# Performance work log

Measured on AMD Instinct MI355X. Metric: run time of the kernel, lower is better.

The kernel has to match this reference:

```python
import jax, jax.numpy as jnp
import numpy as np

N, C, H, W = 4, 15, 320, 320
FEATS_OUT, KSIZE, PAD, CONV_PAD, K_RBF = 32, 11, 11, 5, 31
VMAX = 1.0


def _fft2c(x):
    # fastMRI-style centered orthonormal 2D FFT on complex array [..., H, W]
    x = jnp.fft.ifftshift(x, axes=(-2, -1))
    x = jnp.fft.fft2(x, axes=(-2, -1), norm='ortho')
    return jnp.fft.fftshift(x, axes=(-2, -1))


def _ifft2c(x):
    x = jnp.fft.ifftshift(x, axes=(-2, -1))
    x = jnp.fft.ifft2(x, axes=(-2, -1), norm='ortho')
    return jnp.fft.fftshift(x, axes=(-2, -1))


def _to_c(x):
    return jax.lax.complex(x[..., 0], x[..., 1])


def _to_r(z):
    return jnp.stack([jnp.real(z), jnp.imag(z)], axis=-1)


def setup_inputs() -> dict:
    key = jax.random.key(0)
    ks = jax.random.split(key, 8)
    u_t = jax.random.normal(ks[0], (N, H, W, 2), dtype=jnp.float32)
    f = jax.random.normal(ks[1], (N, C, H, W, 2), dtype=jnp.float32)
    coil_sens = jax.random.normal(ks[2], (N, C, H, W, 2), dtype=jnp.float32)
    sampling_mask = (jax.random.uniform(ks[3], (N, H, W)) < 0.35).astype(jnp.float32)
    conv_kernel = jax.random.normal(ks[4], (FEATS_OUT, 1, KSIZE, KSIZE, 2), dtype=jnp.float32)
    conv_kernel = conv_kernel / np.sqrt(KSIZE * KSIZE * 2 * 1)
    conv_kernel = conv_kernel - jnp.mean(conv_kernel, axis=(1, 2, 3, 4), keepdims=True)
    x0 = jnp.linspace(-VMAX, VMAX, K_RBF, dtype=jnp.float32)
    w = jnp.broadcast_to((0.04 * x0).reshape(1, 1, 1, 1, K_RBF), (1, FEATS_OUT, 1, 1, K_RBF)).astype(jnp.float32)
    mu = x0
    sigma = jnp.array([2.0 * VMAX / (K_RBF - 1)], dtype=jnp.float32)
    lamb = jnp.array([1.0], dtype=jnp.float32)
    return {'u_t': u_t, 'f': f, 'coil_sens': coil_sens, 'sampling_mask': sampling_mask,
            'conv_kernel': conv_kernel, 'w': w, 'mu': mu, 'sigma': sigma, 'lamb': lamb}


def reference(u_t, f, coil_sens, sampling_mask, conv_kernel, w, mu, sigma, lamb):
    dn = ('NCHW', 'OIHW', 'NCHW')
    feats_out = conv_kernel.shape[0]
    k = conv_kernel.shape[2]

    # --- regularizer: reflect-pad, complex conv pair, RBF activation, transposed conv pair ---
    pad_cfg = ((0, 0), (0, 0), (PAD, PAD), (PAD, PAD))
    ur = jnp.pad(u_t[:, None, :, :, 0], pad_cfg, mode='reflect')  # [N,1,Hp,Wp]
    ui = jnp.pad(u_t[:, None, :, :, 1], pad_cfg, mode='reflect')

    def conv(x, Wk):
        return jax.lax.conv_general_dilated(x, Wk, (1, 1), [(CONV_PAD, CONV_PAD)] * 2,
                                            dimension_numbers=dn)

    u_k = conv(ur, conv_kernel[..., 0]) + conv(ui, conv_kernel[..., 1])  # [N,Co,Hp,Wp]

    # RBF activation: sum_i w_i * exp(-(x - mu_i)^2 / (2 sigma^2)), scanned over centers
    wk = jnp.transpose(w[0, :, 0, 0, :])  # [K, Co]
    inv2s2 = 1.0 / (2.0 * sigma[0] ** 2)

    def body(acc, wm):
        wi, mi = wm
        acc = acc + wi[None, :, None, None] * jnp.exp(-jnp.square(u_k - mi) * inv2s2)
        return acc, None

    f_u_k, _ = jax.lax.scan(body, jnp.zeros_like(u_k), (wk, mu))

    # conv_transpose2d(padding=CONV_PAD) == conv with flipped kernel, swapped channels, padding k-1-CONV_PAD
    tpad = k - 1 - CONV_PAD

    def convT(x, Wk):
        Wt = jnp.transpose(Wk[:, :, ::-1, ::-1], (1, 0, 2, 3))  # [I,O,k,k] -> OIHW w/ O=1
        return jax.lax.conv_general_dilated(x, Wt, (1, 1), [(tpad, tpad)] * 2,
                                            dimension_numbers=dn)

    Ru_r = convT(f_u_k, conv_kernel[..., 0])[:, 0]  # [N,Hp,Wp]
    Ru_i = convT(f_u_k, conv_kernel[..., 1])[:, 0]
    Ru = jnp.stack([Ru_r, Ru_i], axis=-1)[:, PAD:-PAD, PAD:-PAD, :] / feats_out  # [N,H,W,2]

    # --- data consistency: A^T (A u - f) (cartesian, os=False) ---
    u_c = _to_c(u_t)              # [N,H,W]
    c_c = _to_c(coil_sens)        # [N,C,H,W]
    f_c = _to_c(f)                # [N,C,H,W]
    m = sampling_mask[:, None]    # [N,1,H,W]
    Au = m * _fft2c(u_c[:, None] * c_c)
    At = jnp.sum(_ifft2c(m * (Au - f_c)) * jnp.conj(c_c), axis=1)  # [N,H,W]
    Du = _to_r(At) * lamb[0]

    return u_t - Ru - Du
```

## Files before the change

### kernel.cpp

```cpp
#include <hip/hip_runtime.h>
#include <hip/hip_bf16.h>
#include <math.h>

#define NN 4
#define CC 15
#define HH 320
#define WW 320
#define HW (HH*WW)
#define FF 32
#define KS 11
#define PADN 11
#define CPAD 5
#define HP 342
#define NK 31
#define NCB (NN*CC)

typedef short bf16x8 __attribute__((ext_vector_type(8)));
typedef float f32x4 __attribute__((ext_vector_type(4)));
typedef unsigned short u16x4 __attribute__((ext_vector_type(4)));

#define MFMA16 __builtin_amdgcn_mfma_f32_16x16x32_bf16

__device__ __forceinline__ unsigned int pack_bf(float r, float i) {
  __hip_bfloat16 hr = __float2bfloat16(r), hi = __float2bfloat16(i);
  unsigned short ur = *(unsigned short*)&hr, ui = *(unsigned short*)&hi;
  return (unsigned int)ur | ((unsigned int)ui << 16);
}
__device__ __forceinline__ unsigned short f2b(float x) {
  __hip_bfloat16 h = __float2bfloat16(x);
  return *(unsigned short*)&h;
}
__device__ __forceinline__ float b2f(unsigned short u) {
  __hip_bfloat16 h = *(__hip_bfloat16*)&u;
  return __bfloat162float(h);
}

__global__ void k_dft(unsigned int* __restrict__ Fbf) {
  int idx = blockIdx.x * blockDim.x + threadIdx.x;
  if (idx >= HW) return;
  int k = idx / WW, n = idx % WW;
  int prod = (k - 160) * (n - 160);
  int r = prod % 320; if (r < 0) r += 320;
  float ang = -6.283185307179586f * (float)r / 320.0f;
  const float s = 0.05590169943749474f;
  Fbf[idx] = pack_bf(cosf(ang) * s, sinf(ang) * s);
}

__global__ void k_prep(const float* __restrict__ ck, unsigned int* __restrict__ Wpk) {
  int idx = blockIdx.x * blockDim.x + threadIdx.x;
  if (idx >= 32 * 176) return;
  int o = idx / 176, kw = idx % 176;
  int ky = kw / 16, kx = kw % 16;
  unsigned int v = 0;
  if (kx <= 10) {
    const float* p = &ck[(o * 121 + ky * 11 + kx) * 2];
    v = pack_bf(p[0], p[1]);
  }
  Wpk[idx] = v;
}

__global__ void k_prep2(const float* __restrict__ ck, unsigned short* __restrict__ Wt) {
  int idx = blockIdx.x * blockDim.x + threadIdx.x;
  if (idx >= 2 * 11 * 16 * 32) return;
  int o = idx & 31;
  int ky = (idx >> 5) & 15;
  int rest = idx >> 9;
  int kx = rest % 11, ch = rest / 11;
  unsigned short v = 0;
  if (ky <= 10) v = f2b(ck[(o * 121 + ky * 11 + kx) * 2 + ch]);
  Wt[idx] = v;
}

__global__ __launch_bounds__(256) void k_conv_rbf_mfma(
    const float* __restrict__ u_t, const unsigned int* __restrict__ Wpk,
    const float* __restrict__ w, const float* __restrict__ mu,
    const float* __restrict__ sigma, unsigned short* __restrict__ fukT) {
  __shared__ unsigned int lW[32 * 180];
  __shared__ unsigned int tIn[26 * 32];
  __shared__ float wl[32 * 36];
  int n = blockIdx.z;
  int y0 = blockIdx.y * 16, x0 = blockIdx.x * 16;
  int tid = threadIdx.x;
  for (int i = tid; i < 32 * 176; i += 256)
    lW[(i / 176) * 180 + (i % 176)] = Wpk[i];
  for (int i = tid; i < 32 * 36; i += 256) {
    int idx = i % 36;
    wl[i] = (idx < 31) ? w[(i / 36) * 31 + idx] : 0.f;
  }
  for (int i = tid; i < 26 * 32; i += 256) {
    int rr = i >> 5, cc = i & 31;
    unsigned int v = 0;
    if (cc < 26) {
      int py = y0 + rr - 5, px = x0 + cc - 5;
      if (py >= 0 && py < HP && px >= 0 && px < HP) {
        int uy = py - PADN; uy = uy < 0 ? -uy : (uy >= HH ? 2 * (HH - 1) - uy : uy);
        int ux = px - PADN; ux = ux < 0 ? -ux : (ux >= WW ? 2 * (WW - 1) - ux : ux);
        const float* up = &u_t[((n * HH + uy) * WW + ux) * 2];
        v = pack_bf(up[0], up[1]);
      }
    }
    tIn[i] = v;
  }
  __syncthreads();
  int lane = tid & 63, wave = tid >> 6;
  int m16 = lane & 15, kq = lane >> 4;
  const short* lWs = (const short*)lW;
  f32x4 acc[4][2] = {};
  for (int ky = 0; ky < 11; ky++) {
    bf16x8 af0 = *(const bf16x8*)&lWs[m16 * 360 + ky * 32 + kq * 8];
    bf16x8 af1 = *(const bf16x8*)&lWs[(m16 + 16) * 360 + ky * 32 + kq * 8];
    #pragma unroll
    for (int nt = 0; nt < 4; nt++) {
      int rr = wave * 4 + nt + ky;
      int c0 = rr * 32 + m16 + kq * 4;
      union { unsigned int u[4]; bf16x8 v; } bu;
      bu.u[0] = tIn[c0]; bu.u[1] = tIn[c0 + 1];
      bu.u[2] = tIn[c0 + 2]; bu.u[3] = tIn[c0 + 3];
      acc[nt][0] = MFMA16(af0, bu.v, acc[nt][0], 0, 0, 0);
      acc[nt][1] = MFMA16(af1, bu.v, acc[nt][1], 0, 0, 0);
    }
  }
  float mu0 = mu[0];
  float dmu = mu[1] - mu[0];
  float invD = 1.0f / dmu;
  float sg = sigma[0];
  float nInv = -1.0f / (2.0f * sg * sg);
  #pragma unroll
  for (int nt = 0; nt < 4; nt++) {
    int Y = y0 + wave * 4 + nt;
    int X = x0 + m16;
    if (Y >= HP || X >= HP) continue;
    #pragma unroll
    for (int mt = 0; mt < 2; mt++) {
      u16x4 pk;
      #pragma unroll
      for (int r = 0; r < 4; r++) {
        float v = acc[nt][mt][r];
        int o = mt * 16 + kq * 4 + r;
        float cf = fminf(fmaxf(rintf((v - mu0) * invD), 0.f), 30.f);
        int i0a = ((int)cf - 5) & ~3;
        if (i0a < 0) i0a = 0; if (i0a > 20) i0a = 20;
        const f32x4* wp = (const f32x4*)&wl[o * 36 + i0a];
        f32x4 w0 = wp[0], w1 = wp[1], w2 = wp[2];
        float base = mu0 + (float)i0a * dmu;
        float res = 0.f;
        #pragma unroll
        for (int ii = 0; ii < 12; ii++) {
          float d = v - (base + (float)ii * dmu);
          float wv = (ii < 4) ? w0[ii] : (ii < 8) ? w1[ii - 4] : w2[ii - 8];
          res += wv * __expf(d * d * nInv);
        }
        pk[r] = f2b(res);
      }
      *(u16x4*)&fukT[(((size_t)n * HP + Y) * HP + X) * 32 + mt * 16 + kq * 4] = pk;
    }
  }
}

__global__ __launch_bounds__(256) void k_convT_mfma(
    const unsigned short* __restrict__ fukT, const unsigned short* __restrict__ Wt,
    float* __restrict__ Ru) {
  __shared__ unsigned short rowBuf[42 * 32];
  __shared__ float accS[16 * 67];
  int n = blockIdx.z;
  int y0 = blockIdx.y * 16, x0 = blockIdx.x * 32;
  int tid = threadIdx.x;
  int lane = tid & 63, wave = tid >> 6;
  int ch = wave >> 1, xh = wave & 1;
  int m16 = lane & 15, kq = lane >> 4;
  bf16x8 afr[11];
  #pragma unroll
  for (int kx = 0; kx < 11; kx++)
    afr[kx] = *(const bf16x8*)&Wt[((ch * 11 + kx) * 16 + m16) * 32 + kq * 8];
  for (int i = tid; i < 16 * 67; i += 256) accS[i] = 0.f;
  int xl = xh * 16 + m16;
  for (int t = 0; t < 26; t++) {
    int r = y0 + 6 + t;
    __syncthreads();
    {
      const unsigned int* src = (const unsigned int*)&fukT[(((size_t)n * HP + r) * HP + x0 + 6) * 32];
      unsigned int* dst = (unsigned int*)rowBuf;
      for (int i = tid; i < 42 * 16; i += 256) dst[i] = src[i];
    }
    __syncthreads();
    f32x4 dacc = {};
    #pragma unroll
    for (int kx = 0; kx < 11; kx++) {
      bf16x8 bfrag = *(const bf16x8*)&rowBuf[(xl + 10 - kx) * 32 + kq * 8];
      dacc = MFMA16(afr[kx], bfrag, dacc, 0, 0, 0);
    }
    #pragma unroll
    for (int rg = 0; rg < 4; rg++) {
      int ky = kq * 4 + rg;
      int y = t + ky - 10;
      if (ky <= 10 && y >= 0 && y < 16)
        accS[y * 67 + xl * 2 + ch] += dacc[rg];
    }
  }
  __syncthreads();
  int chO = tid & 1, xO = (tid >> 1) & 31, yb = tid >> 6;
  #pragma unroll
  for (int q = 0; q < 4; q++) {
    int y = yb + q * 4;
    Ru[(((size_t)n * HH + y0 + y) * WW + x0 + xO) * 2 + chO] = accS[y * 67 + xO * 2 + chO];
  }
}

__global__ void k_umul(const float* __restrict__ u_t, const float* __restrict__ cs,
                       unsigned int* __restrict__ X0) {
  int idx = blockIdx.x * blockDim.x + threadIdx.x;
  if (idx >= NCB * HW) return;
  int hw = idx % HW;
  int n = (idx / HW) / CC;
  float ur = u_t[(n * HW + hw) * 2], ui = u_t[(n * HW + hw) * 2 + 1];
  float cr = cs[idx * 2], ci = cs[idx * 2 + 1];
  X0[idx] = pack_bf(ur * cr - ui * ci, ur * ci + ui * cr);
}

__global__ __launch_bounds__(256) void k_gemm(
    const unsigned int* __restrict__ Abase, long aStride,
    unsigned int xorA1, unsigned int xorA2,
    const unsigned int* __restrict__ Bbase, long bStride, unsigned int xorB,
    unsigned int* __restrict__ OutB, int mode,
    const float* __restrict__ mask, const float* __restrict__ fdat) {
  __shared__ unsigned int lA1[64 * 20], lA2[64 * 20], lB[64 * 20];
  int b = blockIdx.z;
  int i0 = blockIdx.y * 64, j0 = blockIdx.x * 64;
  const unsigned int* A = Abase + (size_t)b * aStride;
  const unsigned int* B = Bbase + (size_t)b * bStride;
  int tid = threadIdx.x;
  int lane = tid & 63, wave = tid >> 6;
  int wy = (wave >> 1) * 32, wx = (wave & 1) * 32;
  int m16 = lane & 15, kq = lane >> 4;
  f32x4 accR[2][2] = {}, accI[2][2] = {};
  int ar = tid >> 4, akc = tid & 15;
  int bj = tid & 63, bk0 = tid >> 6;
  const short* lA1s = (const short*)lA1;
  const short* lA2s = (const short*)lA2;
  const short* lBs  = (const short*)lB;
  for (int kc0 = 0; kc0 < WW; kc0 += 16) {
    __syncthreads();
    #pragma unroll
    for (int it = 0; it < 4; it++) {
      int r = ar + 16 * it;
      unsigned int p = A[(i0 + r) * WW + kc0 + akc];
      lA1[r * 20 + akc] = p ^ xorA1;
      lA2[r * 20 + akc] = ((p >> 16) | (p << 16)) ^ xorA2;
    }
    #pragma unroll
    for (int it = 0; it < 4; it++) {
      int kc = bk0 + 4 * it;
      unsigned int p = B[(kc0 + kc) * WW + j0 + bj];
      lB[bj * 20 + kc] = p ^ xorB;
    }
    __syncthreads();
    bf16x8 a1[2], a2[2], bb[2];
    #pragma unroll
    for (int d = 0; d < 2; d++) {
      int row = wy + d * 16 + m16;
      a1[d] = *(const bf16x8*)&lA1s[row * 40 + kq * 8];
      a2[d] = *(const bf16x8*)&lA2s[row * 40 + kq * 8];
      int col = wx + d * 16 + m16;
      bb[d] = *(const bf16x8*)&lBs[col * 40 + kq * 8];
    }
    #pragma unroll
    for (int di = 0; di < 2; di++)
      #pragma unroll
      for (int dj = 0; dj < 2; dj++) {
        accR[di][dj] = MFMA16(a1[di], bb[dj], accR[di][dj], 0, 0, 0);
        accI[di][dj] = MFMA16(a2[di], bb[dj], accI[di][dj], 0, 0, 0);
      }
  }
  int n = b / CC;
  #pragma unroll
  for (int di = 0; di < 2; di++)
    #pragma unroll
    for (int dj = 0; dj < 2; dj++)
      #pragma unroll
      for (int r = 0; r < 4; r++) {
        int row = i0 + wy + di * 16 + kq * 4 + r;
        int col = j0 + wx + dj * 16 + m16;
        float vr = accR[di][dj][r], vi = accI[di][dj][r];
        size_t idx = (size_t)b * HW + row * WW + col;
        if (mode == 1) {
          float m = mask[n * HW + row * WW + col];
          vr = m * (vr - fdat[idx * 2]);
          vi = m * (vi - fdat[idx * 2 + 1]);
        }
        OutB[idx] = pack_bf(vr, vi);
      }
}

__global__ void k_coilsum(const unsigned int* __restrict__ Z, const float* __restrict__ cs,
                          float* __restrict__ At) {
  int idx = blockIdx.x * blockDim.x + threadIdx.x;
  if (idx >= NN * HW) return;
  int n = idx / HW, hw = idx % HW;
  float ar = 0.f, ai = 0.f;
  for (int c = 0; c < CC; c++) {
    size_t zi = (size_t)(n * CC + c) * HW + hw;
    unsigned int p = Z[zi];
    float zr = b2f((unsigned short)(p & 0xffff));
    float zim = b2f((unsigned short)(p >> 16));
    float crr = cs[zi * 2], cii = cs[zi * 2 + 1];
    ar += zr * crr + zim * cii;
    ai += zim * crr - zr * cii;
  }
  At[idx * 2] = ar;
  At[idx * 2 + 1] = ai;
}

__global__ void k_final(const float* __restrict__ u_t, const float* __restrict__ Ru,
                        const float* __restrict__ At, const float* __restrict__ lamb,
                        float* __restrict__ out) {
  int idx = blockIdx.x * blockDim.x + threadIdx.x;
  if (idx >= NN * HW * 2) return;
  out[idx] = u_t[idx] - Ru[idx] * (1.0f / (float)FF) - lamb[0] * At[idx];
}

extern "C" void kernel_launch(void* const* d_in, const int* in_sizes, int n_in,
                              void* d_out, int out_size, void* d_ws, size_t ws_size,
                              hipStream_t stream) {
  const float* u_t   = (const float*)d_in[0];
  const float* fdat  = (const float*)d_in[1];
  const float* cs    = (const float*)d_in[2];
  const float* mask  = (const float*)d_in[3];
  const float* ck    = (const float*)d_in[4];
  const float* w     = (const float*)d_in[5];
  const float* mu    = (const float*)d_in[6];
  const float* sigma = (const float*)d_in[7];
  const float* lamb  = (const float*)d_in[8];
  float* out = (float*)d_out;

  unsigned int* wsw = (unsigned int*)d_ws;
  unsigned int* Fbf = wsw;
  unsigned int* Wpk = wsw + 102400;
  unsigned short* Wt = (unsigned short*)(wsw + 108160);
  float* At = (float*)(wsw + 113792);
  float* Ru = (float*)(wsw + 932992);
  unsigned int* big = wsw + 1752192;
  unsigned short* fukT = (unsigned short*)big;
  unsigned int* P = big;
  unsigned int* Q = big + 6144000;

  k_dft<<<(HW + 255) / 256, 256, 0, stream>>>(Fbf);
  k_prep<<<(32 * 176 + 255) / 256, 256, 0, stream>>>(ck, Wpk);
  k_prep2<<<(2 * 11 * 16 * 32 + 255) / 256, 256, 0, stream>>>(ck, Wt);
  k_conv_rbf_mfma<<<dim3(22, 22, NN), 256, 0, stream>>>(u_t, Wpk, w, mu, sigma, fukT);
  k_convT_mfma<<<dim3(10, 20, NN), 256, 0, stream>>>(fukT, Wt, Ru);
  k_umul<<<(NCB * HW + 255) / 256, 256, 0, stream>>>(u_t, cs, P);
  k_gemm<<<dim3(5, 5, NCB), 256, 0, stream>>>(Fbf, 0L, 0x80000000u, 0u,
                                              P, (long)HW, 0u,
                                              Q, 0, nullptr, nullptr);
  k_gemm<<<dim3(5, 5, NCB), 256, 0, stream>>>(Q, (long)HW, 0x80000000u, 0u,
                                              Fbf, 0L, 0u,
                                              P, 1, mask, fdat);
  k_gemm<<<dim3(5, 5, NCB), 256, 0, stream>>>(Fbf, 0L, 0u, 0x00008000u,
                                              P, (long)HW, 0u,
                                              Q, 0, nullptr, nullptr);
  k_gemm<<<dim3(5, 5, NCB), 256, 0, stream>>>(Q, (long)HW, 0x80000000u, 0u,
                                              Fbf, 0L, 0x80000000u,
                                              P, 0, nullptr, nullptr);
  k_coilsum<<<(NN * HW + 255) / 256, 256, 0, stream>>>(P, cs, At);
  k_final<<<(NN * HW * 2 + 255) / 256, 256, 0, stream>>>(u_t, Ru, At, lamb, out);
}
```

Measured before the change: 434.4 us.

## Vectorize GEMM tile loads, double K-chunk, prefetch next tile into registers

Reworks the complex-DFT GEMM main loop so global loads are 128-bit vectors and each iteration covers 32 K values instead of 16. The next tile is prefetched into registers while the current one is consumed, overlapping global latency with MFMA work. A single shared A tile replaces the separate real and swapped copies, with the XOR and rotate now applied at LDS-read time, and B is stored K-major. The costs are scalar strided LDS reads for B, extra ALU work per fragment, and higher register pressure.

```diff
diff --git a/kernel.cpp b/kernel.cpp
--- a/kernel.cpp
+++ b/kernel.cpp
@@ -33,6 +33,9 @@
 __device__ __forceinline__ float b2f(unsigned short u) {
   __hip_bfloat16 h = *(__hip_bfloat16*)&u;
   return __bfloat162float(h);
+}
+__device__ __forceinline__ unsigned int rot16(unsigned int x) {
+  return (x >> 16) | (x << 16);
 }
 
 __global__ void k_dft(unsigned int* __restrict__ Fbf) {
@@ -223,7 +226,8 @@
     const unsigned int* __restrict__ Bbase, long bStride, unsigned int xorB,
     unsigned int* __restrict__ OutB, int mode,
     const float* __restrict__ mask, const float* __restrict__ fdat) {
-  __shared__ unsigned int lA1[64 * 20], lA2[64 * 20], lB[64 * 20];
+  __shared__ unsigned int lA[64 * 36];
+  __shared__ unsigned int lB[32 * 68];
   int b = blockIdx.z;
   int i0 = blockIdx.y * 64, j0 = blockIdx.x * 64;
   const unsigned int* A = Abase + (size_t)b * aStride;
@@ -233,43 +237,57 @@
   int wy = (wave >> 1) * 32, wx = (wave & 1) * 32;
   int m16 = lane & 15, kq = lane >> 4;
   f32x4 accR[2][2] = {}, accI[2][2] = {};
-  int ar = tid >> 4, akc = tid & 15;
-  int bj = tid & 63, bk0 = tid >> 6;
-  const short* lA1s = (const short*)lA1;
-  const short* lA2s = (const short*)lA2;
-  const short* lBs  = (const short*)lB;
-  for (int kc0 = 0; kc0 < WW; kc0 += 16) {
+  int ar = tid >> 3;
+  int ag = tid & 7;
+  int bkc = tid >> 4;
+  int bc = (tid & 15) * 4;
+  uint4 pa0, pa1, pb0, pb1;
+  pa0 = *(const uint4*)&A[(i0 + ar) * WW + ag * 4];
+  pa1 = *(const uint4*)&A[(i0 + ar + 32) * WW + ag * 4];
+  pb0 = *(const uint4*)&B[bkc * WW + j0 + bc];
+  pb1 = *(const uint4*)&B[(bkc + 16) * WW + j0 + bc];
+  for (int it = 0; it < 10; it++) {
     __syncthreads();
-    #pragma unroll
-    for (int it = 0; it < 4; it++) {
-      int r = ar + 16 * it;
-      unsigned int p = A[(i0 + r) * WW + kc0 + akc];
-      lA1[r * 20 + akc] = p ^ xorA1;
-      lA2[r * 20 + akc] = ((p >> 16) | (p << 16)) ^ xorA2;
-    }
-    #pragma unroll
-    for (int it = 0; it < 4; it++) {
-      int kc = bk0 + 4 * it;
-      unsigned int p = B[(kc0 + kc) * WW + j0 + bj];
-      lB[bj * 20 + kc] = p ^ xorB;
-    }
+    *(uint4*)&lA[ar * 36 + ag * 4] = pa0;
+    *(uint4*)&lA[(ar + 32) * 36 + ag * 4] = pa1;
+    *(uint4*)&lB[bkc * 68 + bc] = pb0;
+    *(uint4*)&lB[(bkc + 16) * 68 + bc] = pb1;
     __syncthreads();
-    bf16x8 a1[2], a2[2], bb[2];
-    #pragma unroll
-    for (int d = 0; d < 2; d++) {
-      int row = wy + d * 16 + m16;
-      a1[d] = *(const bf16x8*)&lA1s[row * 40 + kq * 8];
-      a2[d] = *(const bf16x8*)&lA2s[row * 40 + kq * 8];
-      int col = wx + d * 16 + m16;
-      bb[d] = *(const bf16x8*)&lBs[col * 40 + kq * 8];
-    }
-    #pragma unroll
-    for (int di = 0; di < 2; di++)
+    if (it < 9) {
+      int kc0 = (it + 1) * 32;
+      pa0 = *(const uint4*)&A[(i0 + ar) * WW + kc0 + ag * 4];
+      pa1 = *(const uint4*)&A[(i0 + ar + 32) * WW + kc0 + ag * 4];
+      pb0 = *(const uint4*)&B[(kc0 + bkc) * WW + j0 + bc];
+      pb1 = *(const uint4*)&B[(kc0 + bkc + 16) * WW + j0 + bc];
+    }
+    #pragma unroll
+    for (int s = 0; s < 2; s++) {
+      bf16x8 a1[2], a2[2], bb[2];
       #pragma unroll
-      for (int dj = 0; dj < 2; dj++) {
-        accR[di][dj] = MFMA16(a1[di], bb[dj], accR[di][dj], 0, 0, 0);
-        accI[di][dj] = MFMA16(a2[di], bb[dj], accI[di][dj], 0, 0, 0);
+      for (int d = 0; d < 2; d++) {
+        int row = wy + d * 16 + m16;
+        uint4 p = *(const uint4*)&lA[row * 36 + s * 16 + kq * 4];
+        union { unsigned int u[4]; bf16x8 v; } ua, ur2, ub;
+        ua.u[0] = p.x ^ xorA1; ua.u[1] = p.y ^ xorA1;
+        ua.u[2] = p.z ^ xorA1; ua.u[3] = p.w ^ xorA1;
+        a1[d] = ua.v;
+        ur2.u[0] = rot16(p.x) ^ xorA2; ur2.u[1] = rot16(p.y) ^ xorA2;
+        ur2.u[2] = rot16(p.z) ^ xorA2; ur2.u[3] = rot16(p.w) ^ xorA2;
+        a2[d] = ur2.v;
+        int col = wx + d * 16 + m16;
+        #pragma unroll
+        for (int j2 = 0; j2 < 4; j2++)
+          ub.u[j2] = lB[(s * 16 + kq * 4 + j2) * 68 + col] ^ xorB;
+        bb[d] = ub.v;
       }
+      #pragma unroll
+      for (int di = 0; di < 2; di++)
+        #pragma unroll
+        for (int dj = 0; dj < 2; dj++) {
+          accR[di][dj] = MFMA16(a1[di], bb[dj], accR[di][dj], 0, 0, 0);
+          accI[di][dj] = MFMA16(a2[di], bb[dj], accI[di][dj], 0, 0, 0);
+        }
+    }
   }
   int n = b / CC;
   #pragma unroll
```

After: 386.8 us. -10.9%, faster.
